# Kernel optimization log

Hardware: AMD Instinct MI355X
Metric: run time of the kernel (lower is better)

## Reference

```python
import jax, jax.numpy as jnp
import numpy as np

N = 50000   # total nodes
E = 800000  # total edges (avg degree 16)
D = 128     # input_dim == hidden_dim
G = 256     # graphs in batch
C = 16      # output classes
L = 5       # num_layers
BN_EPS = 1e-5


def setup_inputs() -> dict:
    key = jax.random.key(0)
    ks = jax.random.split(key, 8)
    s = 1.0 / np.sqrt(D)
    return {
        "x": jax.random.normal(ks[0], (N, D), dtype=jnp.float32),
        "eps": jnp.zeros((L - 1,), dtype=jnp.float32),
        "W1": jax.random.normal(ks[1], (L - 1, D, D), dtype=jnp.float32) * s,
        "b1": jnp.zeros((L - 1, D), dtype=jnp.float32),
        "g1": jnp.ones((L - 1, D), dtype=jnp.float32),
        "beta1": jnp.zeros((L - 1, D), dtype=jnp.float32),
        "W2": jax.random.normal(ks[2], (L - 1, D, D), dtype=jnp.float32) * s,
        "b2": jnp.zeros((L - 1, D), dtype=jnp.float32),
        "g2": jnp.ones((L - 1, D), dtype=jnp.float32),
        "beta2": jnp.zeros((L - 1, D), dtype=jnp.float32),
        "Wp": jax.random.normal(ks[3], (L, D, C), dtype=jnp.float32) * s,
        "bp": jnp.zeros((L, C), dtype=jnp.float32),
        "edge_src": jax.random.randint(ks[4], (E,), 0, N),
        "edge_dst": jax.random.randint(ks[5], (E,), 0, N),
        "graph_ids": jnp.sort(jax.random.randint(ks[6], (N,), 0, G)),
    }


def _bn(x, g, b):
    # BatchNorm1d in training mode: biased batch statistics over the node axis
    m = jnp.mean(x, axis=0)
    v = jnp.mean(jnp.square(x - m), axis=0)
    return g * (x - m) * jax.lax.rsqrt(v + BN_EPS) + b


def reference(x, eps, W1, b1, g1, beta1, W2, b2, g2, beta2, Wp, bp,
              edge_src, edge_dst, graph_ids):
    hidden_representations = [x]
    h = x
    for l in range(L - 1):
        # spmm(adj, h): gather neighbor features along edges, scatter-add to dst
        pooled = jax.ops.segment_sum(h[edge_src], edge_dst, num_segments=N)
        pooled = pooled + (1.0 + eps[l]) * h  # learn_eps branch
        # MLP (num_mlp_layers=2): Linear+BN+ReLU, then Linear
        z = jax.nn.relu(_bn(pooled @ W1[l] + b1[l], g1[l], beta1[l]))
        z = z @ W2[l] + b2[l]
        # outer BN + ReLU
        h = jax.nn.relu(_bn(z, g2[l], beta2[l]))
        hidden_representations.append(h)

    out = jnp.zeros((G, C), dtype=x.dtype)
    for l, hl in enumerate(hidden_representations):
        # graph_pool spmm: sum-pool node features per graph
        pooled_h = jax.ops.segment_sum(hl, graph_ids, num_segments=G)
        out = out + pooled_h @ Wp[l] + bp[l]  # dropout p=0 -> identity
    return out
```

## Files before the change

### kernel.cpp

```cpp
#include <hip/hip_runtime.h>

#define N_NODES  50000
#define N_EDGES  800000
#define DIM      128
#define N_GRAPHS 256
#define N_CLASSES 16
#define N_LAYERS 5
#define BN_EPS   1e-5f

#define GEMM_BM 64
#define LDSP 136

typedef short bf16x8 __attribute__((ext_vector_type(8)));
typedef float f32x4  __attribute__((ext_vector_type(4)));

__device__ __forceinline__ float bf2f(unsigned short u) {
    unsigned int x = ((unsigned int)u) << 16;
    return __builtin_bit_cast(float, x);
}
__device__ __forceinline__ unsigned short f2bf(float f) {
    unsigned int x = __builtin_bit_cast(unsigned int, f);
    x += 0x7fffu + ((x >> 16) & 1u);
    return (unsigned short)(x >> 16);
}
__device__ __forceinline__ float lo16(unsigned int v) { return bf2f((unsigned short)(v & 0xffffu)); }
__device__ __forceinline__ float hi16(unsigned int v) { return bf2f((unsigned short)(v >> 16)); }
__device__ __forceinline__ unsigned int pack16(float a, float b) {
    return (unsigned int)f2bf(a) | ((unsigned int)f2bf(b) << 16);
}


__global__ void deg_kernel(const int* __restrict__ dst, int* __restrict__ deg, int e_count) {
    int e = blockIdx.x * blockDim.x + threadIdx.x;
    if (e < e_count) atomicAdd(&deg[dst[e]], 1);
}

__global__ void fill_csr_kernel(const int* __restrict__ src, const int* __restrict__ dst,
                                int* __restrict__ cursor, int* __restrict__ csr, int e_count) {
    int e = blockIdx.x * blockDim.x + threadIdx.x;
    if (e < e_count) {
        int d = dst[e];
        int p = atomicAdd(&cursor[d], 1);
        csr[p] = src[e];
    }
}

__global__ void gbound_kernel(const int* __restrict__ gid, int* __restrict__ gptr, int n, int G) {
    int i = blockIdx.x * blockDim.x + threadIdx.x;
    if (i >= n) return;
    int cur = gid[i];
    int prev = (i == 0) ? -1 : gid[i - 1];
    for (int g = prev + 1; g <= cur; ++g) gptr[g] = i;
    if (i == n - 1) {
        for (int g = cur + 1; g <= G; ++g) gptr[g] = n;
    }
}


__global__ __launch_bounds__(1024) void scan_part_kernel(const int* __restrict__ in,
                                                         int* __restrict__ part, int n) {
    __shared__ int red[16];
    int tid = threadIdx.x;
    int i = blockIdx.x * 1024 + tid;
    int v = (i < n) ? in[i] : 0;
#pragma unroll
    for (int d = 1; d < 64; d <<= 1) v += __shfl_xor(v, d, 64);
    int lane = tid & 63, w = tid >> 6;
    if (lane == 0) red[w] = v;
    __syncthreads();
    if (tid == 0) {
        int s = 0;
#pragma unroll
        for (int k = 0; k < 16; ++k) s += red[k];
        part[blockIdx.x] = s;
    }
}

__global__ void scan_mid_kernel(int* __restrict__ part, int nb,
                                int* __restrict__ total_out, int total_idx) {
    int lane = threadIdx.x;
    int orig = (lane < nb) ? part[lane] : 0;
    int v = orig;
#pragma unroll
    for (int d = 1; d < 64; d <<= 1) {
        int t = __shfl_up(v, d, 64);
        if (lane >= d) v += t;
    }
    if (lane < nb) part[lane] = v - orig;
    if (lane == 63) total_out[total_idx] = v;
}

__global__ __launch_bounds__(1024) void scan_final_kernel(const int* __restrict__ in,
                                                          const int* __restrict__ part,
                                                          int* __restrict__ rowptr,
                                                          int* __restrict__ cursor, int n) {
    __shared__ int woff[16];
    int tid = threadIdx.x;
    int i = blockIdx.x * 1024 + tid;
    int v = (i < n) ? in[i] : 0;
    int lane = tid & 63, w = tid >> 6;
    int x = v;
#pragma unroll
    for (int d = 1; d < 64; d <<= 1) {
        int t = __shfl_up(x, d, 64);
        if (lane >= d) x += t;
    }
    if (lane == 63) woff[w] = x;
    __syncthreads();
    if (tid == 0) {
        int s = 0;
#pragma unroll
        for (int k = 0; k < 16; ++k) { int t = woff[k]; woff[k] = s; s += t; }
    }
    __syncthreads();
    int excl = part[blockIdx.x] + woff[w] + x - v;
    if (i < n) { rowptr[i] = excl; cursor[i] = excl; }
}


__global__ void f2b_kernel(const float* __restrict__ in, unsigned short* __restrict__ outp, int n4) {
    int i = blockIdx.x * blockDim.x + threadIdx.x;
    if (i >= n4) return;
    float4 v = ((const float4*)in)[i];
    unsigned int a = pack16(v.x, v.y);
    unsigned int b = pack16(v.z, v.w);
    ((uint2*)outp)[i] = make_uint2(a, b);
}

__global__ void wconv_kernel(const float* __restrict__ W, unsigned short* __restrict__ Wt, int nmat) {
    int t = blockIdx.x * blockDim.x + threadIdx.x;
    if (t >= nmat * DIM * DIM) return;
    int m = t >> 14;
    int rem = t & 16383;
    int k = rem >> 7;
    int c = rem & 127;
    Wt[((size_t)m << 14) + (size_t)c * DIM + k] = f2bf(W[t]);
}


__device__ __forceinline__ void gemm_core8(
    unsigned short (*As)[LDSP], const unsigned short* __restrict__ Wt,
    unsigned short* __restrict__ Z, float* __restrict__ colsum, float* __restrict__ colsumsq,
    int nrows, int row0, int tid)
{
    int wid = tid >> 6, lane = tid & 63;
    int mq = wid & 3, ch = wid >> 2;
    int m0 = mq * 16;
    int lrow = lane & 15;
    int lk = (lane >> 4) * 8;

    f32x4 acc[4];
#pragma unroll
    for (int n = 0; n < 4; ++n) acc[n] = (f32x4){0.f, 0.f, 0.f, 0.f};

#pragma unroll
    for (int kk = 0; kk < 4; ++kk) {
        int k0 = kk * 32;
        bf16x8 a = *(const bf16x8*)&As[m0 + lrow][k0 + lk];
#pragma unroll
        for (int n = 0; n < 4; ++n) {
            bf16x8 b = *(const bf16x8*)(Wt + (size_t)(ch * 64 + n * 16 + lrow) * DIM + k0 + lk);
            acc[n] = __builtin_amdgcn_mfma_f32_16x16x32_bf16(a, b, acc[n], 0, 0, 0);
        }
    }

    int r0 = row0 + m0 + (lane >> 4) * 4;
    float sarr[4], qarr[4];
#pragma unroll
    for (int n = 0; n < 4; ++n) {
        int col = ch * 64 + n * 16 + lrow;
        float s = 0.f, q = 0.f;
#pragma unroll
        for (int j = 0; j < 4; ++j) {
            float v = acc[n][j];
            int row = r0 + j;
            if (row < nrows) Z[(size_t)row * DIM + col] = f2bf(v);
            s += v; q += v * v;
        }
        s += __shfl_xor(s, 16); q += __shfl_xor(q, 16);
        s += __shfl_xor(s, 32); q += __shfl_xor(q, 32);
        sarr[n] = s; qarr[n] = q;
    }

    __syncthreads();
    float* red = (float*)&As[0][0];
    if (lane < 16) {
#pragma unroll
        for (int n = 0; n < 4; ++n) {
            int col = ch * 64 + n * 16 + lrow;
            red[wid * 256 + col]       = sarr[n];
            red[wid * 256 + 128 + col] = qarr[n];
        }
    }
    __syncthreads();
    if (tid < 128) {
        int col = tid;
        int base = (col >> 6) * 4 * 256;
        float ts = red[base + col] + red[base + 256 + col]
                 + red[base + 512 + col] + red[base + 768 + col];
        float tq = red[base + 128 + col] + red[base + 384 + col]
                 + red[base + 640 + col] + red[base + 896 + col];
        atomicAdd(&colsum[col], ts);
        atomicAdd(&colsumsq[col], tq);
    }
}


__global__ __launch_bounds__(512) void gemmA_kernel(
    const unsigned short* __restrict__ h, const int* __restrict__ rowptr,
    const int* __restrict__ csr, const float* __restrict__ epsArr, int l,
    const unsigned short* __restrict__ Wt, unsigned short* __restrict__ Z,
    float* __restrict__ stats, int nrows)
{
    __shared__ __attribute__((aligned(16))) unsigned short As[GEMM_BM][LDSP];
    int tid = threadIdx.x;
    int row0 = blockIdx.x * GEMM_BM;
    int wid = tid >> 6, lane = tid & 63;
    int sub = lane >> 4, chunk = lane & 15;
    float ep = 1.0f + epsArr[l];

    for (int i = 0; i < 8; ++i) {
        int node = row0 + wid * 8 + i;
        float a8[8];
#pragma unroll
        for (int j = 0; j < 8; ++j) a8[j] = 0.f;
        if (node < nrows) {
            int beg = rowptr[node], end = rowptr[node + 1];
            int e = beg;
            for (; e + 16 <= end; e += 16) {
                int s0 = csr[e + sub];
                int s1 = csr[e + 4 + sub];
                int s2 = csr[e + 8 + sub];
                int s3 = csr[e + 12 + sub];
                bf16x8 v0 = *(const bf16x8*)(h + (size_t)s0 * DIM + chunk * 8);
                bf16x8 v1 = *(const bf16x8*)(h + (size_t)s1 * DIM + chunk * 8);
                bf16x8 v2 = *(const bf16x8*)(h + (size_t)s2 * DIM + chunk * 8);
                bf16x8 v3 = *(const bf16x8*)(h + (size_t)s3 * DIM + chunk * 8);
#pragma unroll
                for (int j = 0; j < 8; ++j)
                    a8[j] += (bf2f((unsigned short)v0[j]) + bf2f((unsigned short)v1[j]))
                           + (bf2f((unsigned short)v2[j]) + bf2f((unsigned short)v3[j]));
            }
            for (; e + 8 <= end; e += 8) {
                int s0 = csr[e + sub];
                int s1 = csr[e + 4 + sub];
                bf16x8 v0 = *(const bf16x8*)(h + (size_t)s0 * DIM + chunk * 8);
                bf16x8 v1 = *(const bf16x8*)(h + (size_t)s1 * DIM + chunk * 8);
#pragma unroll
                for (int j = 0; j < 8; ++j)
                    a8[j] += bf2f((unsigned short)v0[j]) + bf2f((unsigned short)v1[j]);
            }
            for (; e + 4 <= end; e += 4) {
                int s0 = csr[e + sub];
                bf16x8 v0 = *(const bf16x8*)(h + (size_t)s0 * DIM + chunk * 8);
#pragma unroll
                for (int j = 0; j < 8; ++j) a8[j] += bf2f((unsigned short)v0[j]);
            }
            int rmn = end - e;
            if (sub < rmn) {
                int s0 = csr[e + sub];
                bf16x8 v0 = *(const bf16x8*)(h + (size_t)s0 * DIM + chunk * 8);
#pragma unroll
                for (int j = 0; j < 8; ++j) a8[j] += bf2f((unsigned short)v0[j]);
            }
#pragma unroll
            for (int j = 0; j < 8; ++j) {
                a8[j] += __shfl_xor(a8[j], 16);
                a8[j] += __shfl_xor(a8[j], 32);
            }
            bf16x8 hv = *(const bf16x8*)(h + (size_t)node * DIM + chunk * 8);
#pragma unroll
            for (int j = 0; j < 8; ++j) a8[j] += ep * bf2f((unsigned short)hv[j]);
        }
        if (sub == 0) {
            bf16x8 o;
#pragma unroll
            for (int j = 0; j < 8; ++j) o[j] = (short)f2bf(a8[j]);
            *(bf16x8*)&As[wid * 8 + i][chunk * 8] = o;
        }
    }
    __syncthreads();
    gemm_core8(As, Wt, Z, stats, stats + 128, nrows, row0, tid);
}


__global__ __launch_bounds__(512) void gemmB_kernel(
    const unsigned short* __restrict__ Zin, const float* __restrict__ statsIn,
    const float* __restrict__ g, const float* __restrict__ beta,
    const unsigned short* __restrict__ Wt, unsigned short* __restrict__ Zout,
    float* __restrict__ statsOut, int nrows)
{
    __shared__ __attribute__((aligned(16))) unsigned short As[GEMM_BM][LDSP];
    __shared__ float abn[DIM], shbn[DIM];
    int tid = threadIdx.x;
    int row0 = blockIdx.x * GEMM_BM;

    if (tid < DIM) {
        const float invN = 1.0f / (float)N_NODES;
        float m = statsIn[tid] * invN;
        float var = statsIn[128 + tid] * invN - m * m;
        float s = g[tid] * rsqrtf(var + BN_EPS);
        abn[tid] = s;
        shbn[tid] = beta[tid] - s * m;
    }
    __syncthreads();

#pragma unroll
    for (int it = 0; it < 2; ++it) {
        int c = tid + it * 512;
        int r = c >> 4, kc = c & 15;
        bf16x8 o = {0, 0, 0, 0, 0, 0, 0, 0};
        if (row0 + r < nrows) {
            bf16x8 v = *(const bf16x8*)(Zin + (size_t)(row0 + r) * DIM + kc * 8);
#pragma unroll
            for (int cc = 0; cc < 8; ++cc) {
                int col = kc * 8 + cc;
                float f = bf2f((unsigned short)v[cc]);
                f = fmaxf(fmaf(abn[col], f, shbn[col]), 0.f);
                o[cc] = (short)f2bf(f);
            }
        }
        *(bf16x8*)&As[r][kc * 8] = o;
    }
    __syncthreads();
    gemm_core8(As, Wt, Zout, statsOut, statsOut + 128, nrows, row0, tid);
}


__global__ __launch_bounds__(256) void bnpool_kernel(
    const unsigned short* __restrict__ Zin, const float* __restrict__ stats,
    const float* __restrict__ g, const float* __restrict__ beta,
    const int* __restrict__ gid, unsigned short* __restrict__ hout,
    float* __restrict__ pooled, int nrows)
{
    __shared__ float abn[DIM], shbn[DIM];
    int tid = threadIdx.x;
    if (tid < DIM) {
        const float invN = 1.0f / (float)N_NODES;
        float m = stats[tid] * invN;
        float var = stats[128 + tid] * invN - m * m;
        float s = g[tid] * rsqrtf(var + BN_EPS);
        abn[tid] = s;
        shbn[tid] = beta[tid] - s * m;
    }
    __syncthreads();

    int row0 = blockIdx.x * GEMM_BM;
    int lane = tid & 63, w = tid >> 6;
    int c0 = lane * 2;
    float a0 = abn[c0], a1 = abn[c0 + 1], s0 = shbn[c0], s1 = shbn[c0 + 1];
    const unsigned int* Z2 = (const unsigned int*)Zin;
    unsigned int* H2 = (unsigned int*)hout;

    float px = 0.f, py = 0.f;
    int gcur = -1;
    for (int i = 0; i < 16; ++i) {
        int r = row0 + w * 16 + i;
        if (r >= nrows) break;
        int gg = gid[r];
        if (gg != gcur) {
            if (gcur >= 0) {
                atomicAdd(&pooled[(size_t)gcur * DIM + c0], px);
                atomicAdd(&pooled[(size_t)gcur * DIM + c0 + 1], py);
            }
            gcur = gg; px = 0.f; py = 0.f;
        }
        unsigned int v = Z2[(size_t)r * 64 + lane];
        float f0 = fmaxf(fmaf(a0, lo16(v), s0), 0.f);
        float f1 = fmaxf(fmaf(a1, hi16(v), s1), 0.f);
        unsigned int o = pack16(f0, f1);
        H2[(size_t)r * 64 + lane] = o;
        px += lo16(o);
        py += hi16(o);
    }
    if (gcur >= 0) {
        atomicAdd(&pooled[(size_t)gcur * DIM + c0], px);
        atomicAdd(&pooled[(size_t)gcur * DIM + c0 + 1], py);
    }
}


__global__ __launch_bounds__(256) void pool_kernel(
    const float* __restrict__ h, const int* __restrict__ gptr, float* __restrict__ outp)
{
    __shared__ float red[DIM];
    int g = blockIdx.x;
    int c = threadIdx.x & 127;
    int half = threadIdx.x >> 7;
    int beg = gptr[g], end = gptr[g + 1];
    float acc = 0.f;
    for (int n = beg + half; n < end; n += 2) acc += h[(size_t)n * DIM + c];
    if (half == 1) red[c] = acc;
    __syncthreads();
    if (half == 0) outp[(size_t)g * DIM + c] = acc + red[c];
}


__global__ __launch_bounds__(256) void final_kernel(
    const float* __restrict__ pooledH, const float* __restrict__ Wp,
    const float* __restrict__ bp, float* __restrict__ outp)
{
    int t = blockIdx.x * blockDim.x + threadIdx.x;
    if (t >= N_GRAPHS * N_CLASSES) return;
    int g = t >> 4, c = t & 15;
    float acc = 0.f;
    for (int l = 0; l < N_LAYERS; ++l) {
        const float* ph = pooledH + ((size_t)l * N_GRAPHS + g) * DIM;
        const float* w = Wp + (size_t)l * DIM * N_CLASSES + c;
        float a = 0.f;
        for (int k = 0; k < DIM; ++k) a = fmaf(ph[k], w[k * N_CLASSES], a);
        acc += a + bp[l * N_CLASSES + c];
    }
    outp[t] = acc;
}


extern "C" void kernel_launch(void* const* d_in, const int* in_sizes, int n_in,
                              void* d_out, int out_size, void* d_ws, size_t ws_size,
                              hipStream_t stream) {
    const float* x     = (const float*)d_in[0];
    const float* eps   = (const float*)d_in[1];
    const float* W1    = (const float*)d_in[2];
    const float* g1    = (const float*)d_in[4];
    const float* beta1 = (const float*)d_in[5];
    const float* W2    = (const float*)d_in[6];
    const float* g2    = (const float*)d_in[8];
    const float* beta2 = (const float*)d_in[9];
    const float* Wp    = (const float*)d_in[10];
    const float* bp    = (const float*)d_in[11];
    const int*   esrc  = (const int*)d_in[12];
    const int*   edst  = (const int*)d_in[13];
    const int*   gid   = (const int*)d_in[14];
    float* outp = (float*)d_out;

    char* ws = (char*)d_ws;
    size_t off = 0;
    auto alloc = [&](size_t bytes) {
        char* p = ws + off;
        off = (off + bytes + 255) & ~(size_t)255;
        return p;
    };
    unsigned short* xb  = (unsigned short*)alloc((size_t)N_NODES * DIM * 2);
    unsigned short* B0  = (unsigned short*)alloc((size_t)N_NODES * DIM * 2);
    unsigned short* B1  = (unsigned short*)alloc((size_t)N_NODES * DIM * 2);
    unsigned short* ZB  = (unsigned short*)alloc((size_t)N_NODES * DIM * 2);
    unsigned short* Z2B = (unsigned short*)alloc((size_t)N_NODES * DIM * 2);
    unsigned short* Wt1 = (unsigned short*)alloc((size_t)(N_LAYERS - 1) * DIM * DIM * 2);
    unsigned short* Wt2 = (unsigned short*)alloc((size_t)(N_LAYERS - 1) * DIM * DIM * 2);
    int*   csr     = (int*)alloc((size_t)N_EDGES * 4);
    int*   deg     = (int*)alloc((N_NODES + 1) * 4);
    int*   rowptr  = (int*)alloc((N_NODES + 1) * 4);
    int*   cursor  = (int*)alloc((N_NODES + 1) * 4);
    int*   part    = (int*)alloc(64 * 4);
    int*   growptr = (int*)alloc(300 * 4);
    float* stats   = (float*)alloc(8 * 256 * 4);
    float* pooledH = (float*)alloc((size_t)N_LAYERS * N_GRAPHS * DIM * 4);

    hipMemsetAsync(deg, 0, N_NODES * 4, stream);
    hipMemsetAsync(stats, 0, 8 * 256 * 4, stream);
    hipMemsetAsync(pooledH, 0, (size_t)N_LAYERS * N_GRAPHS * DIM * 4, stream);

    const int nsb = (N_NODES + 1023) / 1024;
    deg_kernel<<<(N_EDGES + 255) / 256, 256, 0, stream>>>(edst, deg, N_EDGES);
    scan_part_kernel<<<nsb, 1024, 0, stream>>>(deg, part, N_NODES);
    scan_mid_kernel<<<1, 64, 0, stream>>>(part, nsb, rowptr, N_NODES);
    scan_final_kernel<<<nsb, 1024, 0, stream>>>(deg, part, rowptr, cursor, N_NODES);
    fill_csr_kernel<<<(N_EDGES + 255) / 256, 256, 0, stream>>>(esrc, edst, cursor, csr, N_EDGES);
    gbound_kernel<<<(N_NODES + 255) / 256, 256, 0, stream>>>(gid, growptr, N_NODES, N_GRAPHS);

    f2b_kernel<<<(N_NODES * DIM / 4 + 255) / 256, 256, 0, stream>>>(x, xb, N_NODES * DIM / 4);
    wconv_kernel<<<((N_LAYERS - 1) * DIM * DIM + 255) / 256, 256, 0, stream>>>(W1, Wt1, N_LAYERS - 1);
    wconv_kernel<<<((N_LAYERS - 1) * DIM * DIM + 255) / 256, 256, 0, stream>>>(W2, Wt2, N_LAYERS - 1);

    pool_kernel<<<N_GRAPHS, 256, 0, stream>>>(x, growptr, pooledH);

    const int ngrid = (N_NODES + GEMM_BM - 1) / GEMM_BM;
    unsigned short* hb = xb;
    unsigned short* nb = B0;
    for (int l = 0; l < N_LAYERS - 1; ++l) {
        gemmA_kernel<<<ngrid, 512, 0, stream>>>(
            hb, rowptr, csr, eps, l, Wt1 + (size_t)l * DIM * DIM, ZB,
            stats + (size_t)(2 * l) * 256, N_NODES);
        gemmB_kernel<<<ngrid, 512, 0, stream>>>(
            ZB, stats + (size_t)(2 * l) * 256, g1 + l * DIM, beta1 + l * DIM,
            Wt2 + (size_t)l * DIM * DIM, Z2B, stats + (size_t)(2 * l + 1) * 256, N_NODES);
        bnpool_kernel<<<ngrid, 256, 0, stream>>>(
            Z2B, stats + (size_t)(2 * l + 1) * 256, g2 + l * DIM, beta2 + l * DIM,
            gid, nb, pooledH + (size_t)(l + 1) * N_GRAPHS * DIM, N_NODES);

        hb = nb;
        nb = (hb == B0) ? B1 : B0;
    }

    final_kernel<<<(N_GRAPHS * N_CLASSES + 255) / 256, 256, 0, stream>>>(pooledH, Wp, bp, outp);
}
```

Before: 666.8 us.

## Fuse outer BN+ReLU into next layer's gather and merge setup kernels

The outer batch-norm and ReLU are no longer materialized as a separate h buffer. The next layer's gather-aggregate kernel now applies the affine BN and ReLU on the fly to each gathered pre-BN row, and the pooling kernel only reads Z2 and accumulates. Setup kernels are merged: degree counting with graph-boundary detection, and x/W conversions with the layer-0 pooling. This removes a full N×D bf16 write per layer and several launches, at the cost of an extra FMA and max per gathered element, about 16× per node, in the gather. Pooled sums are now taken from unrounded fp32 values instead of the bf16-rounded h.

```diff
diff --git a/kernel.cpp b/kernel.cpp
--- a/kernel.cpp
+++ b/kernel.cpp
@@ -30,9 +30,17 @@
 }
 
 
-__global__ void deg_kernel(const int* __restrict__ dst, int* __restrict__ deg, int e_count) {
-    int e = blockIdx.x * blockDim.x + threadIdx.x;
-    if (e < e_count) atomicAdd(&deg[dst[e]], 1);
+__global__ void degbound_kernel(const int* __restrict__ dst, int* __restrict__ deg,
+                                const int* __restrict__ gid, int* __restrict__ gptr) {
+    int i = blockIdx.x * blockDim.x + threadIdx.x;
+    if (i < N_EDGES) atomicAdd(&deg[dst[i]], 1);
+    if (i < N_NODES) {
+        int cur = gid[i];
+        int prev = (i == 0) ? -1 : gid[i - 1];
+        for (int g = prev + 1; g <= cur; ++g) gptr[g] = i;
+        if (i == N_NODES - 1)
+            for (int g = cur + 1; g <= N_GRAPHS; ++g) gptr[g] = N_NODES;
+    }
 }
 
 __global__ void fill_csr_kernel(const int* __restrict__ src, const int* __restrict__ dst,
@@ -42,17 +50,6 @@
         int d = dst[e];
         int p = atomicAdd(&cursor[d], 1);
         csr[p] = src[e];
-    }
-}
-
-__global__ void gbound_kernel(const int* __restrict__ gid, int* __restrict__ gptr, int n, int G) {
-    int i = blockIdx.x * blockDim.x + threadIdx.x;
-    if (i >= n) return;
-    int cur = gid[i];
-    int prev = (i == 0) ? -1 : gid[i - 1];
-    for (int g = prev + 1; g <= cur; ++g) gptr[g] = i;
-    if (i == n - 1) {
-        for (int g = cur + 1; g <= G; ++g) gptr[g] = n;
     }
 }
 
@@ -118,23 +115,45 @@
 }
 
 
-__global__ void f2b_kernel(const float* __restrict__ in, unsigned short* __restrict__ outp, int n4) {
-    int i = blockIdx.x * blockDim.x + threadIdx.x;
-    if (i >= n4) return;
-    float4 v = ((const float4*)in)[i];
-    unsigned int a = pack16(v.x, v.y);
-    unsigned int b = pack16(v.z, v.w);
-    ((uint2*)outp)[i] = make_uint2(a, b);
-}
-
-__global__ void wconv_kernel(const float* __restrict__ W, unsigned short* __restrict__ Wt, int nmat) {
-    int t = blockIdx.x * blockDim.x + threadIdx.x;
-    if (t >= nmat * DIM * DIM) return;
-    int m = t >> 14;
-    int rem = t & 16383;
-    int k = rem >> 7;
-    int c = rem & 127;
-    Wt[((size_t)m << 14) + (size_t)c * DIM + k] = f2bf(W[t]);
+#define CVT_F2B_BLOCKS 2048
+#define CVT_W_BLOCKS   64
+
+__global__ __launch_bounds__(256) void convert_kernel(
+    const float* __restrict__ x, unsigned short* __restrict__ xb,
+    const float* __restrict__ W1, const float* __restrict__ W2,
+    unsigned short* __restrict__ Wt1, unsigned short* __restrict__ Wt2,
+    const int* __restrict__ gptr, float* __restrict__ pool0)
+{
+    __shared__ float red[DIM];
+    int b = blockIdx.x, tid = threadIdx.x;
+    if (b < N_GRAPHS) {
+        int c = tid & 127;
+        int half = tid >> 7;
+        int beg = gptr[b], end = gptr[b + 1];
+        float acc = 0.f;
+        for (int n = beg + half; n < end; n += 2) acc += x[(size_t)n * DIM + c];
+        if (half == 1) red[c] = acc;
+        __syncthreads();
+        if (half == 0) pool0[(size_t)b * DIM + c] = acc + red[c];
+    } else if (b < N_GRAPHS + CVT_F2B_BLOCKS) {
+        const int total = N_NODES * DIM / 4;
+        const int stride = CVT_F2B_BLOCKS * 256;
+        for (int i = (b - N_GRAPHS) * 256 + tid; i < total; i += stride) {
+            float4 v = ((const float4*)x)[i];
+            ((uint2*)xb)[i] = make_uint2(pack16(v.x, v.y), pack16(v.z, v.w));
+        }
+    } else {
+        const int total = (N_LAYERS - 1) * DIM * DIM;
+        const int stride = CVT_W_BLOCKS * 256;
+        for (int t = (b - N_GRAPHS - CVT_F2B_BLOCKS) * 256 + tid; t < total; t += stride) {
+            int m = t >> 14;
+            int k = (t & 16383) >> 7;
+            int c = t & 127;
+            size_t dstp = ((size_t)m << 14) + (size_t)c * DIM + k;
+            Wt1[dstp] = f2bf(W1[t]);
+            Wt2[dstp] = f2bf(W2[t]);
+        }
+    }
 }
 
 
@@ -206,9 +225,12 @@
 }
 
 
+template<int BN>
 __global__ __launch_bounds__(512) void gemmA_kernel(
-    const unsigned short* __restrict__ h, const int* __restrict__ rowptr,
-    const int* __restrict__ csr, const float* __restrict__ epsArr, int l,
+    const unsigned short* __restrict__ src, const float* __restrict__ bnStats,
+    const float* __restrict__ gBN, const float* __restrict__ betaBN,
+    const int* __restrict__ rowptr, const int* __restrict__ csr,
+    const float* __restrict__ epsArr, int l,
     const unsigned short* __restrict__ Wt, unsigned short* __restrict__ Z,
     float* __restrict__ stats, int nrows)
 {
@@ -219,6 +241,23 @@
     int sub = lane >> 4, chunk = lane & 15;
     float ep = 1.0f + epsArr[l];
 
+    float abn[8], sbn[8];
+    if (BN) {
+        const float invN = 1.0f / (float)N_NODES;
+#pragma unroll
+        for (int cc = 0; cc < 8; ++cc) {
+            int c = chunk * 8 + cc;
+            float m = bnStats[c] * invN;
+            float var = bnStats[128 + c] * invN - m * m;
+            float s = gBN[c] * rsqrtf(var + BN_EPS);
+            abn[cc] = s;
+            sbn[cc] = betaBN[c] - s * m;
+        }
+    }
+
+#define TRN(u, cc) (BN ? fmaxf(fmaf(abn[cc], bf2f((unsigned short)(u)), sbn[cc]), 0.f) \
+                       : bf2f((unsigned short)(u)))
+
     for (int i = 0; i < 8; ++i) {
         int node = row0 + wid * 8 + i;
         float a8[8];
@@ -232,45 +271,44 @@
                 int s1 = csr[e + 4 + sub];
                 int s2 = csr[e + 8 + sub];
                 int s3 = csr[e + 12 + sub];
-                bf16x8 v0 = *(const bf16x8*)(h + (size_t)s0 * DIM + chunk * 8);
-                bf16x8 v1 = *(const bf16x8*)(h + (size_t)s1 * DIM + chunk * 8);
-                bf16x8 v2 = *(const bf16x8*)(h + (size_t)s2 * DIM + chunk * 8);
-                bf16x8 v3 = *(const bf16x8*)(h + (size_t)s3 * DIM + chunk * 8);
+                bf16x8 v0 = *(const bf16x8*)(src + (size_t)s0 * DIM + chunk * 8);
+                bf16x8 v1 = *(const bf16x8*)(src + (size_t)s1 * DIM + chunk * 8);
+                bf16x8 v2 = *(const bf16x8*)(src + (size_t)s2 * DIM + chunk * 8);
+                bf16x8 v3 = *(const bf16x8*)(src + (size_t)s3 * DIM + chunk * 8);
 #pragma unroll
                 for (int j = 0; j < 8; ++j)
-                    a8[j] += (bf2f((unsigned short)v0[j]) + bf2f((unsigned short)v1[j]))
-                           + (bf2f((unsigned short)v2[j]) + bf2f((unsigned short)v3[j]));
+                    a8[j] += (TRN(v0[j], j) + TRN(v1[j], j)) + (TRN(v2[j], j) + TRN(v3[j], j));
             }
             for (; e + 8 <= end; e += 8) {
                 int s0 = csr[e + sub];
                 int s1 = csr[e + 4 + sub];
-                bf16x8 v0 = *(const bf16x8*)(h + (size_t)s0 * DIM + chunk * 8);
-                bf16x8 v1 = *(const bf16x8*)(h + (size_t)s1 * DIM + chunk * 8);
+                bf16x8 v0 = *(const bf16x8*)(src + (size_t)s0 * DIM + chunk * 8);
+                bf16x8 v1 = *(const bf16x8*)(src + (size_t)s1 * DIM + chunk * 8);
 #pragma unroll
                 for (int j = 0; j < 8; ++j)
-                    a8[j] += bf2f((unsigned short)v0[j]) + bf2f((unsigned short)v1[j]);
+                    a8[j] += TRN(v0[j], j) + TRN(v1[j], j);
             }
             for (; e + 4 <= end; e += 4) {
                 int s0 = csr[e + sub];
-                bf16x8 v0 = *(const bf16x8*)(h + (size_t)s0 * DIM + chunk * 8);
-#pragma unroll
-                for (int j = 0; j < 8; ++j) a8[j] += bf2f((unsigned short)v0[j]);
+                bf16x8 v0 = *(const bf16x8*)(src + (size_t)s0 * DIM + chunk * 8);
+#pragma unroll
+                for (int j = 0; j < 8; ++j) a8[j] += TRN(v0[j], j);
             }
             int rmn = end - e;
             if (sub < rmn) {
                 int s0 = csr[e + sub];
-                bf16x8 v0 = *(const bf16x8*)(h + (size_t)s0 * DIM + chunk * 8);
-#pragma unroll
-                for (int j = 0; j < 8; ++j) a8[j] += bf2f((unsigned short)v0[j]);
+                bf16x8 v0 = *(const bf16x8*)(src + (size_t)s0 * DIM + chunk * 8);
+#pragma unroll
+                for (int j = 0; j < 8; ++j) a8[j] += TRN(v0[j], j);
             }
 #pragma unroll
             for (int j = 0; j < 8; ++j) {
                 a8[j] += __shfl_xor(a8[j], 16);
                 a8[j] += __shfl_xor(a8[j], 32);
             }
-            bf16x8 hv = *(const bf16x8*)(h + (size_t)node * DIM + chunk * 8);
-#pragma unroll
-            for (int j = 0; j < 8; ++j) a8[j] += ep * bf2f((unsigned short)hv[j]);
+            bf16x8 hv = *(const bf16x8*)(src + (size_t)node * DIM + chunk * 8);
+#pragma unroll
+            for (int j = 0; j < 8; ++j) a8[j] += ep * TRN(hv[j], j);
         }
         if (sub == 0) {
             bf16x8 o;
@@ -279,6 +317,7 @@
             *(bf16x8*)&As[wid * 8 + i][chunk * 8] = o;
         }
     }
+#undef TRN
     __syncthreads();
     gemm_core8(As, Wt, Z, stats, stats + 128, nrows, row0, tid);
 }
@@ -327,11 +366,10 @@
 }
 
 
-__global__ __launch_bounds__(256) void bnpool_kernel(
+__global__ __launch_bounds__(256) void poolZ_kernel(
     const unsigned short* __restrict__ Zin, const float* __restrict__ stats,
     const float* __restrict__ g, const float* __restrict__ beta,
-    const int* __restrict__ gid, unsigned short* __restrict__ hout,
-    float* __restrict__ pooled, int nrows)
+    const int* __restrict__ gid, float* __restrict__ pooled, int nrows)
 {
     __shared__ float abn[DIM], shbn[DIM];
     int tid = threadIdx.x;
@@ -350,7 +388,6 @@
     int c0 = lane * 2;
     float a0 = abn[c0], a1 = abn[c0 + 1], s0 = shbn[c0], s1 = shbn[c0 + 1];
     const unsigned int* Z2 = (const unsigned int*)Zin;
-    unsigned int* H2 = (unsigned int*)hout;
 
     float px = 0.f, py = 0.f;
     int gcur = -1;
@@ -366,33 +403,13 @@
             gcur = gg; px = 0.f; py = 0.f;
         }
         unsigned int v = Z2[(size_t)r * 64 + lane];
-        float f0 = fmaxf(fmaf(a0, lo16(v), s0), 0.f);
-        float f1 = fmaxf(fmaf(a1, hi16(v), s1), 0.f);
-        unsigned int o = pack16(f0, f1);
-        H2[(size_t)r * 64 + lane] = o;
-        px += lo16(o);
-        py += hi16(o);
+        px += fmaxf(fmaf(a0, lo16(v), s0), 0.f);
+        py += fmaxf(fmaf(a1, hi16(v), s1), 0.f);
     }
     if (gcur >= 0) {
         atomicAdd(&pooled[(size_t)gcur * DIM + c0], px);
         atomicAdd(&pooled[(size_t)gcur * DIM + c0 + 1], py);
     }
-}
-
-
-__global__ __launch_bounds__(256) void pool_kernel(
-    const float* __restrict__ h, const int* __restrict__ gptr, float* __restrict__ outp)
-{
-    __shared__ float red[DIM];
-    int g = blockIdx.x;
-    int c = threadIdx.x & 127;
-    int half = threadIdx.x >> 7;
-    int beg = gptr[g], end = gptr[g + 1];
-    float acc = 0.f;
-    for (int n = beg + half; n < end; n += 2) acc += h[(size_t)n * DIM + c];
-    if (half == 1) red[c] = acc;
-    __syncthreads();
-    if (half == 0) outp[(size_t)g * DIM + c] = acc + red[c];
 }
 
 
@@ -441,10 +458,9 @@
         return p;
     };
     unsigned short* xb  = (unsigned short*)alloc((size_t)N_NODES * DIM * 2);
-    unsigned short* B0  = (unsigned short*)alloc((size_t)N_NODES * DIM * 2);
-    unsigned short* B1  = (unsigned short*)alloc((size_t)N_NODES * DIM * 2);
     unsigned short* ZB  = (unsigned short*)alloc((size_t)N_NODES * DIM * 2);
-    unsigned short* Z2B = (unsigned short*)alloc((size_t)N_NODES * DIM * 2);
+    unsigned short* Z2a = (unsigned short*)alloc((size_t)N_NODES * DIM * 2);
+    unsigned short* Z2b = (unsigned short*)alloc((size_t)N_NODES * DIM * 2);
     unsigned short* Wt1 = (unsigned short*)alloc((size_t)(N_LAYERS - 1) * DIM * DIM * 2);
     unsigned short* Wt2 = (unsigned short*)alloc((size_t)(N_LAYERS - 1) * DIM * DIM * 2);
     int*   csr     = (int*)alloc((size_t)N_EDGES * 4);
@@ -461,35 +477,40 @@
     hipMemsetAsync(pooledH, 0, (size_t)N_LAYERS * N_GRAPHS * DIM * 4, stream);
 
     const int nsb = (N_NODES + 1023) / 1024;
-    deg_kernel<<<(N_EDGES + 255) / 256, 256, 0, stream>>>(edst, deg, N_EDGES);
+    degbound_kernel<<<(N_EDGES + 255) / 256, 256, 0, stream>>>(edst, deg, gid, growptr);
     scan_part_kernel<<<nsb, 1024, 0, stream>>>(deg, part, N_NODES);
     scan_mid_kernel<<<1, 64, 0, stream>>>(part, nsb, rowptr, N_NODES);
     scan_final_kernel<<<nsb, 1024, 0, stream>>>(deg, part, rowptr, cursor, N_NODES);
     fill_csr_kernel<<<(N_EDGES + 255) / 256, 256, 0, stream>>>(esrc, edst, cursor, csr, N_EDGES);
-    gbound_kernel<<<(N_NODES + 255) / 256, 256, 0, stream>>>(gid, growptr, N_NODES, N_GRAPHS);
-
-    f2b_kernel<<<(N_NODES * DIM / 4 + 255) / 256, 256, 0, stream>>>(x, xb, N_NODES * DIM / 4);
-    wconv_kernel<<<((N_LAYERS - 1) * DIM * DIM + 255) / 256, 256, 0, stream>>>(W1, Wt1, N_LAYERS - 1);
-    wconv_kernel<<<((N_LAYERS - 1) * DIM * DIM + 255) / 256, 256, 0, stream>>>(W2, Wt2, N_LAYERS - 1);
-
-    pool_kernel<<<N_GRAPHS, 256, 0, stream>>>(x, growptr, pooledH);
+
+    convert_kernel<<<N_GRAPHS + CVT_F2B_BLOCKS + CVT_W_BLOCKS, 256, 0, stream>>>(
+        x, xb, W1, W2, Wt1, Wt2, growptr, pooledH);
 
     const int ngrid = (N_NODES + GEMM_BM - 1) / GEMM_BM;
-    unsigned short* hb = xb;
-    unsigned short* nb = B0;
+    const unsigned short* srcp = xb;
+    unsigned short* Z2cur = Z2a;
     for (int l = 0; l < N_LAYERS - 1; ++l) {
-        gemmA_kernel<<<ngrid, 512, 0, stream>>>(
-            hb, rowptr, csr, eps, l, Wt1 + (size_t)l * DIM * DIM, ZB,
-            stats + (size_t)(2 * l) * 256, N_NODES);
+        float* statsA = stats + (size_t)(2 * l) * 256;
+        float* statsB = stats + (size_t)(2 * l + 1) * 256;
+        if (l == 0) {
+            gemmA_kernel<0><<<ngrid, 512, 0, stream>>>(
+                srcp, stats, g2, beta2,
+                rowptr, csr, eps, l, Wt1 + (size_t)l * DIM * DIM, ZB, statsA, N_NODES);
+        } else {
+            gemmA_kernel<1><<<ngrid, 512, 0, stream>>>(
+                srcp, stats + (size_t)(2 * l - 1) * 256,
+                g2 + (size_t)(l - 1) * DIM, beta2 + (size_t)(l - 1) * DIM,
+                rowptr, csr, eps, l, Wt1 + (size_t)l * DIM * DIM, ZB, statsA, N_NODES);
+        }
         gemmB_kernel<<<ngrid, 512, 0, stream>>>(
-            ZB, stats + (size_t)(2 * l) * 256, g1 + l * DIM, beta1 + l * DIM,
-            Wt2 + (size_t)l * DIM * DIM, Z2B, stats + (size_t)(2 * l + 1) * 256, N_NODES);
-        bnpool_kernel<<<ngrid, 256, 0, stream>>>(
-            Z2B, stats + (size_t)(2 * l + 1) * 256, g2 + l * DIM, beta2 + l * DIM,
-            gid, nb, pooledH + (size_t)(l + 1) * N_GRAPHS * DIM, N_NODES);
-
-        hb = nb;
-        nb = (hb == B0) ? B1 : B0;
+            ZB, statsA, g1 + (size_t)l * DIM, beta1 + (size_t)l * DIM,
+            Wt2 + (size_t)l * DIM * DIM, Z2cur, statsB, N_NODES);
+        poolZ_kernel<<<ngrid, 256, 0, stream>>>(
+            Z2cur, statsB, g2 + (size_t)l * DIM, beta2 + (size_t)l * DIM,
+            gid, pooledH + (size_t)(l + 1) * N_GRAPHS * DIM, N_NODES);
+
+        srcp = Z2cur;
+        Z2cur = (Z2cur == Z2a) ? Z2b : Z2a;
     }
 
     final_kernel<<<(N_GRAPHS * N_CLASSES + 255) / 256, 256, 0, stream>>>(pooledH, Wp, bp, outp);
```

Result: no change. 679.6 us (+1.9%).
